# Kernel tuning notes

Measured on AMD Instinct MI355X. Metric: run time of the kernel, lower is better.

Reference implementation:

```python
import jax, jax.numpy as jnp
import numpy as np

N, M, D = 16384, 2048, 512


def setup_inputs() -> dict:
    key = jax.random.key(0)
    k1, k2 = jax.random.split(key)
    x = jax.random.normal(k1, (N, D), dtype=jnp.float32)
    centers = jax.random.normal(k2, (M, D), dtype=jnp.float32)
    log_sigmas = jnp.zeros((M,), dtype=jnp.float32)
    return {"x": x, "centers": centers, "log_sigmas": log_sigmas}


def reference(x, centers, log_sigmas):
    x_sq = jnp.sum(x * x, axis=1, keepdims=True)          # [N, 1]
    c_sq = jnp.sum(centers * centers, axis=1)             # [M]
    cross = jnp.einsum("nd,md->nm", x, centers)           # [N, M] GEMM
    d = x_sq + c_sq[None, :] - 2.0 * cross                # [N, M]
    sigmas = jnp.exp(log_sigmas)                          # [M]
    return jnp.exp(-d / (2.0 * sigmas[None, :] ** 2))     # [N, M]
```

## Files before the change

### kernel.cpp

```cpp
#include <hip/hip_runtime.h>
#include <hip/hip_bf16.h>
#include <stdint.h>

#define N_ROWS 16384
#define M_COLS 2048
#define D_DIM  512

typedef __attribute__((ext_vector_type(4))) float f32x4;
typedef __attribute__((ext_vector_type(2))) int   i32x2;
typedef long i64;

#define AS1 __attribute__((address_space(1)))
#define AS3 __attribute__((address_space(3)))

__global__ __launch_bounds__(256) void conv_all(const float* __restrict__ x,
                                                const float* __restrict__ cen,
                                                const float* __restrict__ ls,
                                                unsigned char* __restrict__ xb,
                                                unsigned char* __restrict__ cb,
                                                float* __restrict__ xsq,
                                                float* __restrict__ csq,
                                                float* __restrict__ nsc) {
  const int gr   = blockIdx.x * 4 + (threadIdx.x >> 6);
  const int lane = threadIdx.x & 63;
  const float* src;
  unsigned char* dst;
  float* sq;
  int row;
  bool is_c = (gr >= N_ROWS);
  if (is_c) { row = gr - N_ROWS; src = cen; dst = cb; sq = csq; }
  else      { row = gr;          src = x;   dst = xb; sq = xsq; }

  const float* s = src + (size_t)row * D_DIM + lane * 8;
  f32x4 v0 = *(const f32x4*)s;
  f32x4 v1 = *(const f32x4*)(s + 4);
  float acc = v0.x*v0.x + v0.y*v0.y + v0.z*v0.z + v0.w*v0.w
            + v1.x*v1.x + v1.y*v1.y + v1.z*v1.z + v1.w*v1.w;
  i32x2 o;
  int w0 = __builtin_amdgcn_cvt_pk_fp8_f32(v0.x, v0.y, 0, false);
  w0     = __builtin_amdgcn_cvt_pk_fp8_f32(v0.z, v0.w, w0, true);
  int w1 = __builtin_amdgcn_cvt_pk_fp8_f32(v1.x, v1.y, 0, false);
  w1     = __builtin_amdgcn_cvt_pk_fp8_f32(v1.z, v1.w, w1, true);
  o[0] = w0; o[1] = w1;
  *(i32x2*)(dst + (size_t)row * D_DIM + lane * 8) = o;
  #pragma unroll
  for (int off = 32; off > 0; off >>= 1) acc += __shfl_down(acc, off, 64);
  if (lane == 0) sq[row] = acc;
  if (is_c && lane == 1) nsc[row] = -0.5f * expf(-2.0f * ls[row]);
}

static __device__ __forceinline__ void gl2lds16(const unsigned char* g, unsigned char* l) {
  __builtin_amdgcn_global_load_lds((const AS1 uint32_t*)g, (AS3 uint32_t*)l, 16, 0, 0);
}

__global__ __launch_bounds__(256) void gemm_rbf(const unsigned char* __restrict__ A8,
                                                const unsigned char* __restrict__ B8,
                                                const float* __restrict__ xsq,
                                                const float* __restrict__ csq,
                                                const float* __restrict__ nscale,
                                                float* __restrict__ out) {
  __shared__ unsigned char As0[64 * 128], Bs0[64 * 128];
  __shared__ unsigned char As1[64 * 128], Bs1[64 * 128];

  const int t    = threadIdx.x;
  const int lane = t & 63;
  const int w    = t >> 6;
  const int wr   = w >> 1, wc = w & 1;
  const int rowBase = blockIdx.y * 128;
  const int colBase = blockIdx.x * 128;

  int aOff[2], bOff[2];
  #pragma unroll
  for (int q = 0; q < 2; ++q) {
    const int s    = q * 256 + t;
    const int mr   = s >> 3;
    const int c8   = (s & 7) ^ (mr & 7);
    const int srow = 2 * mr + (c8 >> 2);
    const int skc  = (c8 & 3) * 16;
    aOff[q] = (rowBase + srow) * D_DIM + skc;
    bOff[q] = (colBase + srow) * D_DIM + skc;
  }
  const int ld0 = t * 16, ld1 = 4096 + t * 16;

  f32x4 acc[4][4];
  #pragma unroll
  for (int i = 0; i < 4; ++i)
    #pragma unroll
    for (int j = 0; j < 4; ++j)
      #pragma unroll
      for (int r = 0; r < 4; ++r) acc[i][j][r] = 0.0f;

  const int fr  = lane & 15;
  const int q16 = lane >> 4;
  const int frh = fr >> 1;
  const int c4  = (fr & 1) * 4;
  const int khi = q16 >> 1;
  const int sub = (q16 & 1) * 8;
  const int arB = (wr * 32 + frh) * 128;
  const int brB = (wc * 32 + frh) * 128;

#define STAGE(Ab, Bb, kt) do {                      \
    gl2lds16(A8 + aOff[0] + (kt), (Ab) + ld0);      \
    gl2lds16(A8 + aOff[1] + (kt), (Ab) + ld1);      \
    gl2lds16(B8 + bOff[0] + (kt), (Bb) + ld0);      \
    gl2lds16(B8 + bOff[1] + (kt), (Bb) + ld1);      \
  } while (0)

#define COMPUTE(Ab, Bb) do {                                                  \
    _Pragma("unroll")                                                         \
    for (int ks = 0; ks < 2; ++ks) {                                          \
      const int pc = ((c4 + ks * 2 + khi) ^ frh) * 16 + sub;                  \
      i64 af[4], bfr[4];                                                      \
      _Pragma("unroll")                                                       \
      for (int i = 0; i < 4; ++i)                                             \
        af[i] = *(const i64*)&(Ab)[arB + i * 1024 + pc];                      \
      _Pragma("unroll")                                                       \
      for (int j = 0; j < 4; ++j)                                             \
        bfr[j] = *(const i64*)&(Bb)[brB + j * 1024 + pc];                     \
      _Pragma("unroll")                                                       \
      for (int i = 0; i < 4; ++i)                                             \
        _Pragma("unroll")                                                     \
        for (int j = 0; j < 4; ++j)                                           \
          acc[i][j] = __builtin_amdgcn_mfma_f32_16x16x32_fp8_fp8(             \
              af[i], bfr[j], acc[i][j], 0, 0, 0);                             \
    }                                                                         \
  } while (0)

  STAGE(As0, Bs0, 0);
  __syncthreads();
  #pragma unroll
  for (int kk = 0; kk < 4; ++kk) {
    STAGE(As1, Bs1, kk * 128 + 64);
    COMPUTE(As0, Bs0);
    __syncthreads();
    if (kk < 3) STAGE(As0, Bs0, kk * 128 + 128);
    COMPUTE(As1, Bs1);
    if (kk < 3) __syncthreads();
  }

#undef STAGE
#undef COMPUTE

  const int rq = q16 * 4;
  float xs[4][4];
  #pragma unroll
  for (int i = 0; i < 4; ++i)
    #pragma unroll
    for (int r = 0; r < 4; ++r)
      xs[i][r] = xsq[rowBase + wr * 64 + i * 16 + rq + r];

  #pragma unroll
  for (int j = 0; j < 4; ++j) {
    const int c     = colBase + wc * 64 + j * 16 + fr;
    const float cs  = csq[c];
    const float nsc = nscale[c];
    #pragma unroll
    for (int i = 0; i < 4; ++i) {
      const int r0 = rowBase + wr * 64 + i * 16 + rq;
      #pragma unroll
      for (int r = 0; r < 4; ++r) {
        const float dv = xs[i][r] + cs - 2.0f * acc[i][j][r];
        __builtin_nontemporal_store(__expf(dv * nsc),
                                    &out[(size_t)(r0 + r) * M_COLS + c]);
      }
    }
  }
}

__global__ __launch_bounds__(256) void rbf_fallback(const float* __restrict__ x,
                                                    const float* __restrict__ cen,
                                                    const float* __restrict__ ls,
                                                    float* __restrict__ out) {
  __shared__ float xr[D_DIM];
  const int n = blockIdx.y;
  const int m = blockIdx.x * 256 + threadIdx.x;
  for (int d = threadIdx.x; d < D_DIM; d += 256) xr[d] = x[(size_t)n * D_DIM + d];
  __syncthreads();
  const float* cp = cen + (size_t)m * D_DIM;
  float acc = 0.f;
  for (int d = 0; d < D_DIM; d += 4) {
    f32x4 cv = *(const f32x4*)(cp + d);
    float d0 = xr[d + 0] - cv.x;
    float d1 = xr[d + 1] - cv.y;
    float d2 = xr[d + 2] - cv.z;
    float d3 = xr[d + 3] - cv.w;
    acc += d0 * d0 + d1 * d1 + d2 * d2 + d3 * d3;
  }
  const float nsc = -0.5f * expf(-2.0f * ls[m]);
  out[(size_t)n * M_COLS + m] = __expf(acc * nsc);
}

extern "C" void kernel_launch(void* const* d_in, const int* in_sizes, int n_in,
                              void* d_out, int out_size, void* d_ws, size_t ws_size,
                              hipStream_t stream) {
  const float* x   = (const float*)d_in[0];
  const float* cen = (const float*)d_in[1];
  const float* ls  = (const float*)d_in[2];
  float* out = (float*)d_out;

  const size_t need = (size_t)N_ROWS * D_DIM
                    + (size_t)M_COLS * D_DIM
                    + (size_t)N_ROWS * 4
                    + (size_t)M_COLS * 4
                    + (size_t)M_COLS * 4;

  if (ws_size >= need) {
    char* p = (char*)d_ws;
    unsigned char* xb = (unsigned char*)p; p += (size_t)N_ROWS * D_DIM;
    unsigned char* cb = (unsigned char*)p; p += (size_t)M_COLS * D_DIM;
    float* xsq   = (float*)p; p += (size_t)N_ROWS * 4;
    float* csq   = (float*)p; p += (size_t)M_COLS * 4;
    float* nsc   = (float*)p;

    conv_all<<<(N_ROWS + M_COLS) / 4, 256, 0, stream>>>(x, cen, ls, xb, cb, xsq, csq, nsc);
    dim3 grid(M_COLS / 128, N_ROWS / 128);
    gemm_rbf<<<grid, 256, 0, stream>>>(xb, cb, xsq, csq, nsc, out);
  } else {
    dim3 grid(M_COLS / 256, N_ROWS);
    rbf_fallback<<<grid, 256, 0, stream>>>(x, cen, ls, out);
  }
}
```

Before: 180.7 us.

## Stage RBF epilogue through LDS for coalesced 16-byte output stores and swizzle tiles

```diff
diff --git a/kernel.cpp b/kernel.cpp
--- a/kernel.cpp
+++ b/kernel.cpp
@@ -53,21 +53,27 @@
   __builtin_amdgcn_global_load_lds((const AS1 uint32_t*)g, (AS3 uint32_t*)l, 16, 0, 0);
 }
 
-__global__ __launch_bounds__(256) void gemm_rbf(const unsigned char* __restrict__ A8,
-                                                const unsigned char* __restrict__ B8,
-                                                const float* __restrict__ xsq,
-                                                const float* __restrict__ csq,
-                                                const float* __restrict__ nscale,
-                                                float* __restrict__ out) {
-  __shared__ unsigned char As0[64 * 128], Bs0[64 * 128];
-  __shared__ unsigned char As1[64 * 128], Bs1[64 * 128];
+__global__ __launch_bounds__(256, 4) void gemm_rbf(const unsigned char* __restrict__ A8,
+                                                   const unsigned char* __restrict__ B8,
+                                                   const float* __restrict__ xsq,
+                                                   const float* __restrict__ csq,
+                                                   const float* __restrict__ nscale,
+                                                   float* __restrict__ out) {
+  __shared__ __align__(16) unsigned char smem[32768];
+  unsigned char* const As0 = smem;
+  unsigned char* const Bs0 = smem + 8192;
+  unsigned char* const As1 = smem + 16384;
+  unsigned char* const Bs1 = smem + 24576;
 
   const int t    = threadIdx.x;
   const int lane = t & 63;
   const int w    = t >> 6;
   const int wr   = w >> 1, wc = w & 1;
-  const int rowBase = blockIdx.y * 128;
-  const int colBase = blockIdx.x * 128;
+
+  const int lin = blockIdx.y * 16 + blockIdx.x;
+  const int swz = (lin & 7) * 256 + (lin >> 3);
+  const int rowBase = (swz >> 4) * 128;
+  const int colBase = (swz & 15) * 128;
 
   int aOff[2], bOff[2];
   #pragma unroll
@@ -142,28 +148,49 @@
 #undef COMPUTE
 
   const int rq = q16 * 4;
-  float xs[4][4];
-  #pragma unroll
-  for (int i = 0; i < 4; ++i)
-    #pragma unroll
-    for (int r = 0; r < 4; ++r)
-      xs[i][r] = xsq[rowBase + wr * 64 + i * 16 + rq + r];
-
-  #pragma unroll
-  for (int j = 0; j < 4; ++j) {
-    const int c     = colBase + wc * 64 + j * 16 + fr;
-    const float cs  = csq[c];
-    const float nsc = nscale[c];
-    #pragma unroll
-    for (int i = 0; i < 4; ++i) {
-      const int r0 = rowBase + wr * 64 + i * 16 + rq;
+  unsigned char* const region = smem + wr * 16384;
+  const int ln   = lane & 31;
+  const int rsel = lane >> 5;
+
+  __syncthreads();
+  #pragma unroll
+  for (int p = 0; p < 2; ++p) {
+    float xs2[2][4];
+    #pragma unroll
+    for (int i2 = 0; i2 < 2; ++i2)
       #pragma unroll
-      for (int r = 0; r < 4; ++r) {
-        const float dv = xs[i][r] + cs - 2.0f * acc[i][j][r];
-        __builtin_nontemporal_store(__expf(dv * nsc),
-                                    &out[(size_t)(r0 + r) * M_COLS + c]);
+      for (int r = 0; r < 4; ++r)
+        xs2[i2][r] = xsq[rowBase + wr * 64 + (p * 2 + i2) * 16 + rq + r];
+
+    #pragma unroll
+    for (int j = 0; j < 4; ++j) {
+      const int c     = colBase + wc * 64 + j * 16 + fr;
+      const float cs  = csq[c];
+      const float nsc = nscale[c];
+      const int colb  = (wc * 64 + j * 16 + fr) * 4;
+      #pragma unroll
+      for (int i2 = 0; i2 < 2; ++i2) {
+        const int i = p * 2 + i2;
+        #pragma unroll
+        for (int r = 0; r < 4; ++r) {
+          const int lr = i2 * 16 + rq + r;
+          const float dv = xs2[i2][r] + cs - 2.0f * acc[i][j][r];
+          *(float*)(region + lr * 512 + (colb ^ ((lr & 7) << 4))) = __expf(dv * nsc);
+        }
       }
     }
+    __syncthreads();
+
+    const unsigned char* const src = smem + (w >> 1) * 16384;
+    const int rowHalf = (w & 1) * 16;
+    #pragma unroll
+    for (int s = 0; s < 8; ++s) {
+      const int lr = rowHalf + s * 2 + rsel;
+      f32x4 v = *(const f32x4*)(src + lr * 512 + ((ln * 16) ^ ((lr & 7) << 4)));
+      const int g = rowBase + (w >> 1) * 64 + 32 * p + lr;
+      __builtin_nontemporal_store(v, (f32x4*)(out + (size_t)g * M_COLS + colBase + ln * 4));
+    }
+    if (p == 0) __syncthreads();
   }
 }
 
```

New measurement: 182.9 us. About the same (+1.2%).
